# Kernel tuning notes

Hardware: AMD Instinct MI355X
Metric: run time of the kernel (lower is better)

Reference implementation:

```python
import jax, jax.numpy as jnp
import numpy as np

N = 4096  # output_size
B = 4096  # batch rows
NEG_SLOPE = 0.02


def setup_inputs() -> dict:
    key = jax.random.key(0)
    k1, k2, k3, k4 = jax.random.split(key, 4)
    x = jax.random.normal(k1, (B, N), dtype=jnp.float32)
    W = jax.random.normal(k2, (N, N), dtype=jnp.float32)        # self.weights
    beta = jax.random.normal(k3, (1,), dtype=jnp.float32)       # self.beta (scalar param)
    beta_res = jax.random.normal(k4, (N,), dtype=jnp.float32)   # self.res.beta
    return {"x": x, "W": W, "beta": beta, "beta_res": beta_res}


def reference(x, W, beta, beta_res):
    # wrho = x.unsqueeze(1) * W.expand(B,-1,-1); row_sum = wrho.sum(2)  ==  x @ W.T
    row_sum = jnp.einsum("bj,ij->bi", x, W)                 # [B, N]
    out = jax.nn.relu(1.0 - beta + row_sum)                 # hlogic(1 - beta + row_sum)
    # ResEventually: relu(1 - (beta_res - (x + out))), then LeakyReLU(0.02)
    res = jax.nn.relu(1.0 - (beta_res - (x + out)))
    return jnp.where(res >= 0, res, NEG_SLOPE * res)
```

## Files before the change

### kernel.cpp

```cpp
#include <hip/hip_runtime.h>


#define NDIM 4096

typedef __bf16 bf16x8 __attribute__((ext_vector_type(8)));
typedef float f32x4 __attribute__((ext_vector_type(4)));

__device__ unsigned short f2bf(float f) {
    unsigned int x;
    __builtin_memcpy(&x, &f, 4);
    unsigned int r = x + 0x7FFFu + ((x >> 16) & 1u);
    return (unsigned short)(r >> 16);
}

__device__ unsigned int pack_bf2(float lo, float hi) {
    return (unsigned int)f2bf(lo) | ((unsigned int)f2bf(hi) << 16);
}

__device__ inline void gload16(const uint4* g, unsigned int* l) {
    __builtin_amdgcn_global_load_lds(
        (const __attribute__((address_space(1))) unsigned int*)g,
        (__attribute__((address_space(3))) unsigned int*)l,
        16, 0, 0);
}

__global__ void convert_f32_bf16_kernel(const float* src, unsigned int* dst) {
    const size_t i = ((size_t)blockIdx.x * blockDim.x + threadIdx.x) * 8;
    float4 v0 = *(const float4*)(src + i);
    float4 v1 = *(const float4*)(src + i + 4);
    uint4 u;
    u.x = pack_bf2(v0.x, v0.y);
    u.y = pack_bf2(v0.z, v0.w);
    u.z = pack_bf2(v1.x, v1.y);
    u.w = pack_bf2(v1.z, v1.w);
    *(uint4*)(dst + i / 2) = u;
}

#define BAR()   __builtin_amdgcn_s_barrier()
#define VMCNT(n) asm volatile("s_waitcnt vmcnt(" #n ")" ::: "memory")
#define PRIO(x) __builtin_amdgcn_s_setprio(x)

#define STAGE_A(buf, h, S) do { \
    gload16(Ab4 + (offA[2*(h)]   + (S)*8), &sAU[buf][(2*(h))*2048   + wq]); \
    gload16(Ab4 + (offA[2*(h)+1] + (S)*8), &sAU[buf][(2*(h)+1)*2048 + wq]); \
} while (0)
#define STAGE_B(buf, h, S) do { \
    gload16(Bb4 + (offB[2*(h)]   + (S)*8), &sBU[buf][(2*(h))*2048   + wq]); \
    gload16(Bb4 + (offB[2*(h)+1] + (S)*8), &sBU[buf][(2*(h)+1)*2048 + wq]); \
} while (0)

#define READ_A4(dst, pbuf, mt0) do { \
    _Pragma("unroll") for (int _m = 0; _m < 4; _m++) { \
        dst[_m][0] = (pbuf)[afB + ((mt0) + _m) * 128]; \
        dst[_m][1] = (pbuf)[afB + ((mt0) + _m) * 128 + 64]; } \
} while (0)
#define READ_B2(dst, pbuf, nt0) do { \
    _Pragma("unroll") for (int _n = 0; _n < 2; _n++) { \
        dst[_n][0] = (pbuf)[bfB + ((nt0) + _n) * 128]; \
        dst[_n][1] = (pbuf)[bfB + ((nt0) + _n) * 128 + 64]; } \
} while (0)

#define MM16(afr, bfr, mt0, nt0) do { \
    _Pragma("unroll") for (int _k = 0; _k < 2; _k++) \
    _Pragma("unroll") for (int _m = 0; _m < 4; _m++) \
    _Pragma("unroll") for (int _n = 0; _n < 2; _n++) \
        acc[(mt0)+_m][(nt0)+_n] = __builtin_amdgcn_mfma_f32_16x16x32_bf16( \
            afr[_m][_k], bfr[_n][_k], acc[(mt0)+_m][(nt0)+_n], 0, 0, 0); \
} while (0)

__global__ void __launch_bounds__(512, 2)
ResFCEventuallyLayer_82205674045459_kernel(
    const unsigned int* Xbf, const unsigned int* Wbf,
    const float* X, const float* Bp, const float* Br,
    float* out)
{
    __shared__ __align__(16) unsigned int sAU[2][8192];
    __shared__ __align__(16) unsigned int sBU[2][8192];

    const int t    = threadIdx.x;
    const int lane = t & 63;
    const int wave = t >> 6;
    const int quad = lane >> 4;
    const int l16  = lane & 15;
    const int wm   = wave >> 2;
    const int wn   = wave & 3;
    const int wq   = wave * 256;

    const int bid = blockIdx.x;
    const int swz = ((bid & 7) << 5) | (bid >> 3);
    const int bm0 = (swz >> 4) * 256;
    const int bn0 = (swz & 15) * 256;

    const uint4* Ab4 = (const uint4*)Xbf;
    const uint4* Bb4 = (const uint4*)Wbf;

    int offA[4], offB[4];
#pragma unroll
    for (int rr = 0; rr < 4; rr++) {
        const int p   = rr * 512 + t;
        const int r   = (p >> 2) & 15;
        const int sub = p >> 6;
        const int sr  = sub >> 1, sc = sub & 1;
        const int c8  = (p & 3) ^ (((r >> 3) & 1) << 1);
        const int row = sr * 16 + r;
        const int gc  = sc * 4 + c8;
        offA[rr] = (bm0 + row) * 512 + gc;
        offB[rr] = (bn0 + row) * 512 + gc;
    }

    const int laneByte = l16 * 64 + ((quad * 16) ^ (((l16 >> 3) & 1) << 5));
    const int afB = (wm * 16384 + laneByte) >> 4;
    const int bfB = (wn * 8192  + laneByte) >> 4;

    const bf16x8* pA0 = (const bf16x8*)sAU[0];
    const bf16x8* pA1 = (const bf16x8*)sAU[1];
    const bf16x8* pB0 = (const bf16x8*)sBU[0];
    const bf16x8* pB1 = (const bf16x8*)sBU[1];

    f32x4 acc[8][4];
#pragma unroll
    for (int i = 0; i < 8; i++)
#pragma unroll
        for (int j = 0; j < 4; j++)
#pragma unroll
            for (int r = 0; r < 4; r++)
                acc[i][j][r] = 0.0f;

    bf16x8 af0[4][2], af1[4][2], bf0[2][2], bf1[2][2];

    STAGE_A(0, 0, 0); STAGE_B(0, 0, 0); STAGE_B(0, 1, 0); STAGE_A(0, 1, 0);
    STAGE_A(1, 0, 1); STAGE_B(1, 0, 1); STAGE_B(1, 1, 1);
    VMCNT(6);
    BAR();

    for (int j = 0; j < 32; j++) {
        const int S1 = 2 * j + 1;
        const int S2 = (2 * j + 2) & 63;
        const int S3 = (2 * j + 3) & 63;

        STAGE_A(1, 1, S1);
        READ_A4(af0, pA0, 0); READ_B2(bf0, pB0, 0);
        PRIO(1); MM16(af0, bf0, 0, 0); PRIO(0);
        BAR();
        READ_B2(bf1, pB0, 2);
        PRIO(1); MM16(af0, bf1, 0, 2); PRIO(0);
        BAR();
        STAGE_B(0, 0, S2);
        READ_A4(af1, pA0, 4);
        PRIO(1); MM16(af1, bf1, 4, 2); PRIO(0);
        BAR();
        STAGE_B(0, 1, S2);
        STAGE_A(0, 0, S2);
        PRIO(1); MM16(af1, bf0, 4, 0); PRIO(0);
        VMCNT(6);
        BAR();

        STAGE_A(0, 1, S2);
        READ_A4(af0, pA1, 0); READ_B2(bf0, pB1, 0);
        PRIO(1); MM16(af0, bf0, 0, 0); PRIO(0);
        BAR();
        READ_B2(bf1, pB1, 2);
        PRIO(1); MM16(af0, bf1, 0, 2); PRIO(0);
        BAR();
        STAGE_B(1, 0, S3);
        READ_A4(af1, pA1, 4);
        PRIO(1); MM16(af1, bf1, 4, 2); PRIO(0);
        BAR();
        STAGE_B(1, 1, S3);
        STAGE_A(1, 0, S3);
        PRIO(1); MM16(af1, bf0, 4, 0); PRIO(0);
        VMCNT(6);
        BAR();
    }

    const float one_m_beta = 1.0f - Bp[0];
#pragma unroll
    for (int nt = 0; nt < 4; nt++) {
        const int n = bn0 + wn * 64 + nt * 16 + l16;
        const float br = Br[n];
#pragma unroll
        for (int mt = 0; mt < 8; mt++) {
            const int mbase = bm0 + wm * 128 + mt * 16 + quad * 4;
#pragma unroll
            for (int r = 0; r < 4; r++) {
                const size_t idx = (size_t)(mbase + r) * NDIM + n;
                float v = acc[mt][nt][r] + one_m_beta;
                if (v < 0.0f) v = 0.0f;
                float res = 1.0f - br + X[idx] + v;
                if (res < 0.0f) res = 0.0f;
                out[idx] = res;
            }
        }
    }
}

__global__ void resfc_fallback_kernel(
    const float* X, const float* W,
    const float* Bp, const float* Br,
    float* out)
{
    __shared__ __align__(16) unsigned int sA[128 * 16];
    __shared__ __align__(16) unsigned int sB[128 * 16];

    const int t    = threadIdx.x;
    const int lane = t & 63;
    const int wave = t >> 6;
    const int quad = lane >> 4;
    const int l16  = lane & 15;
    const int wm   = wave >> 1;
    const int wn   = wave & 1;

    const int bm0 = blockIdx.y * 128;
    const int bn0 = blockIdx.x * 128;

    const float* gA[4];
    const float* gB[4];
    int ldsIdx[4];
    for (int c = 0; c < 4; c++) {
        const int ch   = t + c * 256;
        const int row  = ch >> 3;
        const int col4 = ch & 7;
        gA[c] = X + (size_t)(bm0 + row) * NDIM + col4 * 4;
        gB[c] = W + (size_t)(bn0 + row) * NDIM + col4 * 4;
        ldsIdx[c] = row * 16 + col4 * 2;
    }

    typedef __bf16 bf16x8_ __attribute__((ext_vector_type(8)));
    const bf16x8* pa = (const bf16x8*)sA + (wm * 64 + l16) * 4 + quad;
    const bf16x8* pb = (const bf16x8*)sB + (wn * 64 + l16) * 4 + quad;

    f32x4 acc[4][4];
    for (int i = 0; i < 4; i++)
        for (int j = 0; j < 4; j++)
            for (int r = 0; r < 4; r++)
                acc[i][j][r] = 0.0f;

    for (int k0 = 0; k0 < NDIM; k0 += 32) {
        float4 va[4], vb[4];
        for (int c = 0; c < 4; c++) {
            va[c] = *(const float4*)(gA[c] + k0);
            vb[c] = *(const float4*)(gB[c] + k0);
        }
        __syncthreads();
        for (int c = 0; c < 4; c++) {
            uint2 ua, ub;
            ua.x = pack_bf2(va[c].x, va[c].y);
            ua.y = pack_bf2(va[c].z, va[c].w);
            ub.x = pack_bf2(vb[c].x, vb[c].y);
            ub.y = pack_bf2(vb[c].z, vb[c].w);
            *(uint2*)(sA + ldsIdx[c]) = ua;
            *(uint2*)(sB + ldsIdx[c]) = ub;
        }
        __syncthreads();

        bf16x8 af[4], bfr[4];
        for (int mt = 0; mt < 4; mt++) af[mt]  = pa[mt * 64];
        for (int nt = 0; nt < 4; nt++) bfr[nt] = pb[nt * 64];

        for (int mt = 0; mt < 4; mt++)
            for (int nt = 0; nt < 4; nt++)
                acc[mt][nt] = __builtin_amdgcn_mfma_f32_16x16x32_bf16(
                    af[mt], bfr[nt], acc[mt][nt], 0, 0, 0);
    }

    const float one_m_beta = 1.0f - Bp[0];
    for (int nt = 0; nt < 4; nt++) {
        const int n = bn0 + wn * 64 + nt * 16 + l16;
        const float br = Br[n];
        for (int mt = 0; mt < 4; mt++) {
            const int mbase = bm0 + wm * 64 + mt * 16 + quad * 4;
            for (int r = 0; r < 4; r++) {
                const size_t idx = (size_t)(mbase + r) * NDIM + n;
                float v = acc[mt][nt][r] + one_m_beta;
                if (v < 0.0f) v = 0.0f;
                float res = 1.0f - br + X[idx] + v;
                if (res < 0.0f) res = 0.0f;
                out[idx] = res;
            }
        }
    }
}

extern "C" void kernel_launch(void* const* d_in, const int* in_sizes, int n_in,
                              void* d_out, int out_size, void* d_ws, size_t ws_size,
                              hipStream_t stream) {
    (void)in_sizes; (void)n_in; (void)out_size;

    const float* X  = (const float*)d_in[0];
    const float* W  = (const float*)d_in[1];
    const float* Bp = (const float*)d_in[2];
    const float* Br = (const float*)d_in[3];
    float* out      = (float*)d_out;

    const size_t elems   = (size_t)NDIM * NDIM;
    const size_t bf_need = elems * 2 * 2;

    dim3 block(256);

    if (ws_size >= bf_need) {
        unsigned int* Xbf = (unsigned int*)d_ws;
        unsigned int* Wbf = (unsigned int*)d_ws + elems / 2;

        dim3 cvt_grid((unsigned int)(elems / 8 / 256));
        hipLaunchKernelGGL(convert_f32_bf16_kernel, cvt_grid, block, 0, stream, X, Xbf);
        hipLaunchKernelGGL(convert_f32_bf16_kernel, cvt_grid, block, 0, stream, W, Wbf);
        hipLaunchKernelGGL(ResFCEventuallyLayer_82205674045459_kernel,
                           dim3(256), dim3(512), 0, stream, Xbf, Wbf, X, Bp, Br, out);
    } else {
        hipLaunchKernelGGL(resfc_fallback_kernel,
                           dim3(NDIM / 128, NDIM / 128), block, 0, stream,
                           X, W, Bp, Br, out);
    }
}
```

Baseline: 318.5 us.

## Merge conversion launches, drop a barrier, read bf16 X in epilogue

Folds the two fp32-to-bf16 conversion launches into one grid that picks X or W by block index. Inside the GEMM main loop, the first two MFMA groups of each half-iteration now share one LDS read phase and lose a barrier between them. The epilogue reads the bf16 copy of X instead of fp32 X, which halves residual read traffic but adds rounding error to the residual term. Output uses nontemporal stores to limit cache pollution.

```diff
diff --git a/kernel.cpp b/kernel.cpp
--- a/kernel.cpp
+++ b/kernel.cpp
@@ -24,8 +24,14 @@
         16, 0, 0);
 }
 
-__global__ void convert_f32_bf16_kernel(const float* src, unsigned int* dst) {
-    const size_t i = ((size_t)blockIdx.x * blockDim.x + threadIdx.x) * 8;
+__global__ void convert_f32_bf16_kernel(const float* X, unsigned int* Xbf,
+                                        const float* W, unsigned int* Wbf) {
+    unsigned int bid = blockIdx.x;
+    const float* src;
+    unsigned int* dst;
+    if (bid < 8192) { src = X; dst = Xbf; }
+    else            { src = W; dst = Wbf; bid -= 8192; }
+    const size_t i = ((size_t)bid * blockDim.x + threadIdx.x) * 8;
     float4 v0 = *(const float4*)(src + i);
     float4 v1 = *(const float4*)(src + i + 4);
     uint4 u;
@@ -139,11 +145,8 @@
         const int S3 = (2 * j + 3) & 63;
 
         STAGE_A(1, 1, S1);
-        READ_A4(af0, pA0, 0); READ_B2(bf0, pB0, 0);
-        PRIO(1); MM16(af0, bf0, 0, 0); PRIO(0);
-        BAR();
-        READ_B2(bf1, pB0, 2);
-        PRIO(1); MM16(af0, bf1, 0, 2); PRIO(0);
+        READ_A4(af0, pA0, 0); READ_B2(bf0, pB0, 0); READ_B2(bf1, pB0, 2);
+        PRIO(1); MM16(af0, bf0, 0, 0); MM16(af0, bf1, 0, 2); PRIO(0);
         BAR();
         STAGE_B(0, 0, S2);
         READ_A4(af1, pA0, 4);
@@ -156,11 +159,8 @@
         BAR();
 
         STAGE_A(0, 1, S2);
-        READ_A4(af0, pA1, 0); READ_B2(bf0, pB1, 0);
-        PRIO(1); MM16(af0, bf0, 0, 0); PRIO(0);
-        BAR();
-        READ_B2(bf1, pB1, 2);
-        PRIO(1); MM16(af0, bf1, 0, 2); PRIO(0);
+        READ_A4(af0, pA1, 0); READ_B2(bf0, pB1, 0); READ_B2(bf1, pB1, 2);
+        PRIO(1); MM16(af0, bf0, 0, 0); MM16(af0, bf1, 0, 2); PRIO(0);
         BAR();
         STAGE_B(1, 0, S3);
         READ_A4(af1, pA1, 4);
@@ -174,6 +174,7 @@
     }
 
     const float one_m_beta = 1.0f - Bp[0];
+    const unsigned short* Xh = (const unsigned short*)Xbf;
 #pragma unroll
     for (int nt = 0; nt < 4; nt++) {
         const int n = bn0 + wn * 64 + nt * 16 + l16;
@@ -184,14 +185,18 @@
 #pragma unroll
             for (int r = 0; r < 4; r++) {
                 const size_t idx = (size_t)(mbase + r) * NDIM + n;
+                unsigned int xu = (unsigned int)Xh[idx] << 16;
+                float xv;
+                __builtin_memcpy(&xv, &xu, 4);
                 float v = acc[mt][nt][r] + one_m_beta;
                 if (v < 0.0f) v = 0.0f;
-                float res = 1.0f - br + X[idx] + v;
+                float res = 1.0f - br + xv + v;
                 if (res < 0.0f) res = 0.0f;
-                out[idx] = res;
+                __builtin_nontemporal_store(res, &out[idx]);
             }
         }
     }
+    (void)X;
 }
 
 __global__ void resfc_fallback_kernel(
@@ -225,7 +230,6 @@
         ldsIdx[c] = row * 16 + col4 * 2;
     }
 
-    typedef __bf16 bf16x8_ __attribute__((ext_vector_type(8)));
     const bf16x8* pa = (const bf16x8*)sA + (wm * 64 + l16) * 4 + quad;
     const bf16x8* pb = (const bf16x8*)sB + (wn * 64 + l16) * 4 + quad;
 
@@ -295,20 +299,17 @@
     const size_t elems   = (size_t)NDIM * NDIM;
     const size_t bf_need = elems * 2 * 2;
 
-    dim3 block(256);
-
     if (ws_size >= bf_need) {
         unsigned int* Xbf = (unsigned int*)d_ws;
         unsigned int* Wbf = (unsigned int*)d_ws + elems / 2;
 
-        dim3 cvt_grid((unsigned int)(elems / 8 / 256));
-        hipLaunchKernelGGL(convert_f32_bf16_kernel, cvt_grid, block, 0, stream, X, Xbf);
-        hipLaunchKernelGGL(convert_f32_bf16_kernel, cvt_grid, block, 0, stream, W, Wbf);
+        hipLaunchKernelGGL(convert_f32_bf16_kernel, dim3(16384), dim3(256),
+                           0, stream, X, Xbf, W, Wbf);
         hipLaunchKernelGGL(ResFCEventuallyLayer_82205674045459_kernel,
                            dim3(256), dim3(512), 0, stream, Xbf, Wbf, X, Bp, Br, out);
     } else {
         hipLaunchKernelGGL(resfc_fallback_kernel,
-                           dim3(NDIM / 128, NDIM / 128), block, 0, stream,
+                           dim3(NDIM / 128, NDIM / 128), dim3(256), 0, stream,
                            X, W, Bp, Br, out);
     }
 }
```

Measured after the change: 294.7 us. 7.4% less time.
